# Performance work log

Hardware: AMD Instinct MI355X
Metric: run time of the kernel (lower is better)

Reference implementation:

```python
import jax, jax.numpy as jnp
import numpy as np


def _softsplat(tenIn, tenFlow):
    """Bilinear forward splatting: scatter tenIn to flow-displaced locations.
    tenIn: [N,C,H,W], tenFlow: [N,2,H,W] -> out [N,C,H,W]."""
    N, C, H, W = tenIn.shape
    dt = tenIn.dtype
    gx = jnp.arange(W, dtype=dt)[None, None, :]   # [1,1,W]
    gy = jnp.arange(H, dtype=dt)[None, :, None]   # [1,H,1]
    fx = gx + tenFlow[:, 0]                       # [N,H,W] target x
    fy = gy + tenFlow[:, 1]                       # [N,H,W] target y
    finite = jnp.isfinite(fx) & jnp.isfinite(fy)
    x0f = jnp.floor(fx)
    y0f = jnp.floor(fy)
    ix0 = x0f.astype(jnp.int32)
    iy0 = y0f.astype(jnp.int32)
    # bilinear corner weights (NW, NE, SW, SE) exactly as in the CUDA kernel
    wx1 = fx - x0f            # weight toward east
    wx0 = (x0f + 1.0) - fx    # weight toward west
    wy1 = fy - y0f            # weight toward south
    wy0 = (y0f + 1.0) - fy    # weight toward north
    corners = [
        (ix0,     iy0,     wx0 * wy0),  # NW
        (ix0 + 1, iy0,     wx1 * wy0),  # NE
        (ix0,     iy0 + 1, wx0 * wy1),  # SW
        (ix0 + 1, iy0 + 1, wx1 * wy1),  # SE
    ]
    HW = H * W
    tenIn_flat = tenIn.reshape(N, C, HW)

    def scatter_corner(ix, iy, w):
        valid = finite & (ix >= 0) & (ix < W) & (iy >= 0) & (iy < H)
        idx = jnp.where(valid, iy * W + ix, 0).reshape(N, HW)       # [N,HW]
        wv = jnp.where(valid, w, jnp.zeros_like(w)).reshape(N, 1, HW)
        vals = (tenIn_flat * wv).transpose(0, 2, 1)                 # [N,HW,C]
        seg = jax.vmap(lambda v, i: jax.ops.segment_sum(v, i, num_segments=HW))(vals, idx)
        return seg                                                   # [N,HW,C]

    out = scatter_corner(*corners[0])
    for c in corners[1:]:
        out = out + scatter_corner(*c)
    return out.transpose(0, 2, 1).reshape(N, C, H, W)


def softsplat_softmax(tenIn, tenFlow, tenMetric):
    # strMode == 'softmax': splat [tenIn * exp(metric), exp(metric)], then normalize
    w = jnp.exp(tenMetric)                          # [N,1,H,W]
    packed = jnp.concatenate([tenIn * w, w], axis=1)
    out = _softsplat(packed, tenFlow)
    norm = out[:, -1:]
    norm = jnp.where(norm == 0.0, jnp.ones_like(norm), norm)
    return out[:, :-1] / norm


def setup_inputs() -> dict:
    key = jax.random.key(0)
    k1, k2, k3 = jax.random.split(key, 3)
    N, C, H, W = 8, 64, 288, 512
    tenIn = jax.random.normal(k1, (N, C, H, W), dtype=jnp.float32)
    tenFlow = jax.random.normal(k2, (N, 2, H, W), dtype=jnp.float32)
    tenMetric = jax.random.normal(k3, (N, 1, H, W), dtype=jnp.float32)
    return {"tenIn": tenIn, "tenFlow": tenFlow, "tenMetric": tenMetric}


def reference(tenIn, tenFlow, tenMetric):
    return softsplat_softmax(tenIn, tenFlow, tenMetric)
```

## Files before the change

kernel.cpp:

```cpp
#include <hip/hip_runtime.h>
#include <hip/hip_fp16.h>
#include <math.h>

constexpr int N  = 8;
constexpr int C  = 64;
constexpr int H  = 288;
constexpr int W  = 512;
constexpr int HW = H * W;

constexpr int TW = 64, TH = 32, R = 8;
constexpr int PW = TW + 2 * R;
constexpr int PH = TH + 2 * R;
constexpr int PS = PW * PH;
constexpr int TGX = W / TW;
constexpr int TGY = H / TH;
constexpr int TILES = N * TGX * TGY;
constexpr int NOUT = TH * TW;
constexpr int K = 12;
constexpr int CCHB = 4;
constexpr int NCHUNK = C / CCHB;
constexpr int NSPLIT = 2;
constexpr int CPB = NCHUNK / NSPLIT;
constexpr int OVFCAP = 256;
constexpr int ESCCAP = 512;
constexpr int NTC = 512;
constexpr int NTG = 1024;
constexpr int GGRID = TILES * NSPLIT;

constexpr size_t CLAIM_LDS_WORDS = (size_t)NOUT * (K + 1);
constexpr size_t CLAIM_LDS_BYTES = CLAIM_LDS_WORDS * 4;

constexpr size_t WS_DEN  = 0;
constexpr size_t WS_META = WS_DEN  + (size_t)N * HW;
constexpr size_t WS_OVFC = WS_META + (size_t)TILES * NOUT * K;
constexpr size_t WS_OVFE = WS_OVFC + TILES;
constexpr size_t WS_ESCC = WS_OVFE + (size_t)TILES * OVFCAP * 2;
constexpr size_t WS_ESCE = WS_ESCC + TILES;

__device__ __forceinline__ int swz(int si) { return si ^ ((si >> 4) & 15); }

__device__ __forceinline__ unsigned packh2(float a, float b) {
    __half2 h = __floats2half2_rn(a, b);
    return *reinterpret_cast<unsigned*>(&h);
}
__device__ __forceinline__ float2 unpackh2(unsigned u) {
    __half2 h = *reinterpret_cast<__half2*>(&u);
    return __half22float2(h);
}

__global__ __launch_bounds__(NTC) void claim_kernel(
    const float* __restrict__ flow, const float* __restrict__ metric,
    unsigned* __restrict__ meta,
    unsigned* __restrict__ ovfc, unsigned* __restrict__ ovfe,
    unsigned* __restrict__ escc, unsigned* __restrict__ esce,
    float* __restrict__ den)
{
    extern __shared__ unsigned smem[];
    unsigned* cnt = smem;
    unsigned* ml  = smem + NOUT;

    for (int i = threadIdx.x; i < NOUT; i += NTC) cnt[i] = 0;
    for (int i = threadIdx.x; i < NOUT * K; i += NTC) ml[i] = 0u;
    __syncthreads();

    const int t  = blockIdx.x;
    const int n  = t / (TGX * TGY);
    const int r  = t % (TGX * TGY);
    const int Y0 = (r / TGX) * TH;
    const int X0 = (r % TGX) * TW;

    const float* fxp = flow + ((size_t)n * 2) * HW;
    const float* fyp = fxp + HW;
    const float* mp  = metric + (size_t)n * HW;
    unsigned* mt = meta + (size_t)t * NOUT * K;

    for (int si = threadIdx.x; si < PS; si += NTC) {
        int ys = Y0 - R + si / PW;
        int xs = X0 - R + si % PW;
        if ((unsigned)ys >= (unsigned)H || (unsigned)xs >= (unsigned)W) continue;
        int p = ys * W + xs;
        float fx = fxp[p] + (float)xs;
        float fy = fyp[p] + (float)ys;
        if (!(isfinite(fx) && isfinite(fy))) continue;
        float x0f = floorf(fx), y0f = floorf(fy);
        int ix0 = (int)x0f, iy0 = (int)y0f;
        int tx = ix0 - X0;
        int ty = iy0 - Y0;
        float wx1 = fx - x0f, wx0 = x0f + 1.0f - fx;
        float wy1 = fy - y0f, wy0 = y0f + 1.0f - fy;
        float wm  = __expf(mp[p]);
        int sis = swz(si);

        #define CLAIM(TYv, TXv, Wv)                                           \
            if ((unsigned)(TYv) < (unsigned)TH &&                             \
                (unsigned)(TXv) < (unsigned)TW) {                             \
                float w_ = (Wv) * wm;                                         \
                int   o_ = (TYv) * TW + (TXv);                                \
                unsigned slot = atomicAdd(&cnt[o_], 1u);                      \
                if (slot < (unsigned)K) {                                     \
                    ml[o_ * K + (int)slot] =                                  \
                        ((unsigned)__half_as_ushort(__float2half(w_)) << 16)  \
                        | (unsigned)sis;                                      \
                } else {                                                      \
                    unsigned p2 = atomicAdd(&ovfc[t], 1u);                    \
                    if (p2 < (unsigned)OVFCAP) {                              \
                        unsigned* e = ovfe + ((size_t)t * OVFCAP + p2) * 2;   \
                        e[0] = ((unsigned)o_ << 16) | (unsigned)sis;          \
                        e[1] = __float_as_uint(w_);                           \
                    }                                                         \
                }                                                             \
            }
        CLAIM(ty,     tx,     wx0 * wy0)
        CLAIM(ty,     tx + 1, wx1 * wy0)
        CLAIM(ty + 1, tx,     wx0 * wy1)
        CLAIM(ty + 1, tx + 1, wx1 * wy1)
        #undef CLAIM

        if ((unsigned)(xs - X0) < (unsigned)TW &&
            (unsigned)(ys - Y0) < (unsigned)TH) {
            int   cx[4] = { ix0, ix0 + 1, ix0,     ix0 + 1 };
            int   cy[4] = { iy0, iy0,     iy0 + 1, iy0 + 1 };
            float cw[4] = { wx0 * wy0, wx1 * wy0, wx0 * wy1, wx1 * wy1 };
            #pragma unroll
            for (int k = 0; k < 4; ++k) {
                if ((unsigned)cx[k] >= (unsigned)W ||
                    (unsigned)cy[k] >= (unsigned)H) continue;
                int tX0 = cx[k] & ~(TW - 1);
                int tY0 = cy[k] & ~(TH - 1);
                bool inpad = (xs >= tX0 - R) && (xs < tX0 + TW + R) &&
                             (ys >= tY0 - R) && (ys < tY0 + TH + R);
                if (inpad) continue;
                int tt = n * (TGX * TGY) + (tY0 >> 5) * TGX + (tX0 >> 6);
                unsigned pos = atomicAdd(&escc[tt], 1u);
                if (pos < (unsigned)ESCCAP) {
                    unsigned* e = esce + ((size_t)tt * ESCCAP + pos) * 3;
                    e[0] = (unsigned)((cy[k] - tY0) * TW + (cx[k] - tX0));
                    e[1] = (unsigned)p;
                    e[2] = __float_as_uint(cw[k] * wm);
                }
            }
        }
    }
    __syncthreads();

    const unsigned on = min(ovfc[t], (unsigned)OVFCAP);
    const unsigned* oe = ovfe + (size_t)t * OVFCAP * 2;
    for (int o = threadIdx.x; o < NOUT; o += NTC) {
        unsigned cn = min(cnt[o], (unsigned)K);
        float d = 0.0f;
        for (unsigned s = 0; s < cn; ++s)
            d += __half2float(__ushort_as_half(
                     (unsigned short)(ml[o * K + (int)s] >> 16)));
        for (unsigned i = 0; i < on; ++i)
            if ((oe[2 * i] >> 16) == (unsigned)o)
                d += __uint_as_float(oe[2 * i + 1]);
        den[(size_t)n * HW + (Y0 + o / TW) * W + X0 + o % TW] = d;
    }

    const uint4* mlv = reinterpret_cast<const uint4*>(ml);
    uint4* mtv = reinterpret_cast<uint4*>(mt);
    for (int i = threadIdx.x; i < NOUT * K / 4; i += NTC)
        mtv[i] = mlv[i];
}

__global__ __launch_bounds__(NTG, 4) void gather_kernel(
    const float* __restrict__ in, const unsigned* __restrict__ meta,
    const unsigned* __restrict__ ovfc, const unsigned* __restrict__ ovfe,
    const unsigned* __restrict__ escc, const unsigned* __restrict__ esce,
    const float* __restrict__ den, float* __restrict__ out)
{
    __shared__ uint2 val[2][PS];

    const int b0 = blockIdx.x;
    const int b  = (b0 & 7) * (GGRID / 8) + (b0 >> 3);
    const int t     = b >> 1;
    const int split = b & 1;
    const int n  = t / (TGX * TGY);
    const int r  = t % (TGX * TGY);
    const int Y0 = (r / TGX) * TH;
    const int X0 = (r % TGX) * TW;

    const unsigned on = min(ovfc[t], (unsigned)OVFCAP);
    const unsigned en = min(escc[t], (unsigned)ESCCAP);
    const unsigned* oe = ovfe + (size_t)t * OVFCAP * 2;
    const unsigned* ee = esce + (size_t)t * ESCCAP * 3;
    const unsigned* mt = meta + (size_t)t * NOUT * K;

    float inv[2];
    int   opix[2];
    #pragma unroll
    for (int k = 0; k < 2; ++k) {
        int o = threadIdx.x + k * NTG;
        opix[k] = (Y0 + o / TW) * W + X0 + o % TW;
        float d = den[(size_t)n * HW + opix[k]];
        for (unsigned i = 0; i < en; ++i)
            if (ee[3 * i] == (unsigned)o) d += __uint_as_float(ee[3 * i + 2]);
        inv[k] = (d == 0.0f) ? 1.0f : 1.0f / d;
    }

    const bool stager = threadIdx.x < PS / 4;
    int si0 = 0, sw = 0, soff = 0;
    bool ok = false;
    if (stager) {
        si0 = threadIdx.x * 4;
        int row = si0 / PW;
        int ys  = Y0 - R + row;
        int xs0 = X0 - R + (si0 - row * PW);
        ok  = (unsigned)ys < (unsigned)H && (unsigned)xs0 < (unsigned)W;
        sw  = (si0 >> 4) & 15;
        soff = ys * W + xs0;
    }
    const float* inb0 = in + ((size_t)n * C + split * CPB * CCHB) * HW;

    float4 g0 = {0,0,0,0}, g1 = g0, g2 = g0, g3 = g0;
    if (stager && ok) {
        const float* pp = inb0 + soff;
        g0 = *reinterpret_cast<const float4*>(pp);
        g1 = *reinterpret_cast<const float4*>(pp + HW);
        g2 = *reinterpret_cast<const float4*>(pp + 2 * HW);
        g3 = *reinterpret_cast<const float4*>(pp + 3 * HW);
    }
    if (stager) {
        val[0][(si0    ) ^ sw] = make_uint2(packh2(g0.x, g1.x), packh2(g2.x, g3.x));
        val[0][(si0 + 1) ^ sw] = make_uint2(packh2(g0.y, g1.y), packh2(g2.y, g3.y));
        val[0][(si0 + 2) ^ sw] = make_uint2(packh2(g0.z, g1.z), packh2(g2.z, g3.z));
        val[0][(si0 + 3) ^ sw] = make_uint2(packh2(g0.w, g1.w), packh2(g2.w, g3.w));
    }

    int cur = 0;
    for (int cc = 0; cc < CPB; ++cc) {
        __syncthreads();
        const float* inb = inb0 + (size_t)cc * CCHB * HW;

        if (cc + 1 < CPB && stager) {
            g0 = make_float4(0,0,0,0); g1 = g0; g2 = g0; g3 = g0;
            if (ok) {
                const float* pn = inb + (size_t)CCHB * HW + soff;
                g0 = *reinterpret_cast<const float4*>(pn);
                g1 = *reinterpret_cast<const float4*>(pn + HW);
                g2 = *reinterpret_cast<const float4*>(pn + 2 * HW);
                g3 = *reinterpret_cast<const float4*>(pn + 3 * HW);
            }
        }

        const uint2* vb = val[cur];
        #pragma unroll
        for (int k = 0; k < 2; ++k) {
            const int o = threadIdx.x + k * NTG;
            const uint4* mo4 = reinterpret_cast<const uint4*>(mt + (size_t)o * K);
            uint4 qa = mo4[0], qb = mo4[1], qc = mo4[2];
            unsigned mloc[K] = { qa.x, qa.y, qa.z, qa.w,
                                 qb.x, qb.y, qb.z, qb.w,
                                 qc.x, qc.y, qc.z, qc.w };

            float a0 = 0.0f, a1 = 0.0f, a2 = 0.0f, a3 = 0.0f;
            #pragma unroll
            for (int s = 0; s < K; ++s) {
                unsigned m_ = mloc[s];
                float w  = __half2float(__ushort_as_half((unsigned short)(m_ >> 16)));
                uint2 v = vb[m_ & 0xffffu];
                float2 f0 = unpackh2(v.x), f1 = unpackh2(v.y);
                a0 += w * f0.x;  a1 += w * f0.y;
                a2 += w * f1.x;  a3 += w * f1.y;
            }
            for (unsigned i = 0; i < on; ++i) {
                unsigned e0 = oe[2 * i];
                if ((e0 >> 16) == (unsigned)o) {
                    float w  = __uint_as_float(oe[2 * i + 1]);
                    uint2 v = vb[e0 & 0xffffu];
                    float2 f0 = unpackh2(v.x), f1 = unpackh2(v.y);
                    a0 += w * f0.x;  a1 += w * f0.y;
                    a2 += w * f1.x;  a3 += w * f1.y;
                }
            }
            for (unsigned i = 0; i < en; ++i) {
                if (ee[3 * i] == (unsigned)o) {
                    float w  = __uint_as_float(ee[3 * i + 2]);
                    int   ps = (int)ee[3 * i + 1];
                    a0 += w * inb[ps];
                    a1 += w * inb[ps + HW];
                    a2 += w * inb[ps + 2 * HW];
                    a3 += w * inb[ps + 3 * HW];
                }
            }
            size_t ob = ((size_t)n * C + (split * CPB + cc) * CCHB) * HW + opix[k];
            out[ob]          = a0 * inv[k];
            out[ob + HW]     = a1 * inv[k];
            out[ob + 2 * HW] = a2 * inv[k];
            out[ob + 3 * HW] = a3 * inv[k];
        }

        if (cc + 1 < CPB && stager) {
            uint2* vn = val[cur ^ 1];
            vn[(si0    ) ^ sw] = make_uint2(packh2(g0.x, g1.x), packh2(g2.x, g3.x));
            vn[(si0 + 1) ^ sw] = make_uint2(packh2(g0.y, g1.y), packh2(g2.y, g3.y));
            vn[(si0 + 2) ^ sw] = make_uint2(packh2(g0.z, g1.z), packh2(g2.z, g3.z));
            vn[(si0 + 3) ^ sw] = make_uint2(packh2(g0.w, g1.w), packh2(g2.w, g3.w));
        }
        cur ^= 1;
    }
}

extern "C" void kernel_launch(void* const* d_in, const int* in_sizes, int n_in,
                              void* d_out, int out_size, void* d_ws, size_t ws_size,
                              hipStream_t stream)
{
    const float* tenIn     = (const float*)d_in[0];
    const float* tenFlow   = (const float*)d_in[1];
    const float* tenMetric = (const float*)d_in[2];
    float* out = (float*)d_out;

    unsigned* ws  = (unsigned*)d_ws;
    float*    den = (float*)(ws + WS_DEN);
    unsigned* meta = ws + WS_META;
    unsigned* ovfc = ws + WS_OVFC;
    unsigned* ovfe = ws + WS_OVFE;
    unsigned* escc = ws + WS_ESCC;
    unsigned* esce = ws + WS_ESCE;

    hipFuncSetAttribute(reinterpret_cast<const void*>(claim_kernel),
                        hipFuncAttributeMaxDynamicSharedMemorySize,
                        (int)CLAIM_LDS_BYTES);

    hipMemsetAsync(ovfc, 0, TILES * sizeof(unsigned), stream);
    hipMemsetAsync(escc, 0, TILES * sizeof(unsigned), stream);

    claim_kernel<<<TILES, NTC, CLAIM_LDS_BYTES, stream>>>(
        tenFlow, tenMetric, meta, ovfc, ovfe, escc, esce, den);
    gather_kernel<<<GGRID, NTG, 0, stream>>>(tenIn, meta, ovfc, ovfe,
                                             escc, esce, den, out);
}
```

Baseline: 230.1 us.

## Halve gather block size and drop LDS double buffering for occupancy

The gather kernel now runs 512 threads per block instead of 1024, and each thread handles four output pixels instead of two. The double-buffered LDS staging with register prefetch is replaced by a single buffer. Each channel chunk is now staged cooperatively in a loop and bracketed by two barriers. This halves LDS per block and removes the prefetch registers, so more blocks can be resident and hide latency. In exchange, the explicit overlap of global loads for the next chunk with compute on the current one is lost.

```diff
diff --git a/kernel.cpp b/kernel.cpp
--- a/kernel.cpp
+++ b/kernel.cpp
@@ -24,7 +24,8 @@
 constexpr int OVFCAP = 256;
 constexpr int ESCCAP = 512;
 constexpr int NTC = 512;
-constexpr int NTG = 1024;
+constexpr int NTG = 512;
+constexpr int OPT = NOUT / NTG;
 constexpr int GGRID = TILES * NSPLIT;
 
 constexpr size_t CLAIM_LDS_WORDS = (size_t)NOUT * (K + 1);
@@ -169,7 +170,7 @@
     const unsigned* __restrict__ escc, const unsigned* __restrict__ esce,
     const float* __restrict__ den, float* __restrict__ out)
 {
-    __shared__ uint2 val[2][PS];
+    __shared__ uint2 val[PS];
 
     const int b0 = blockIdx.x;
     const int b  = (b0 & 7) * (GGRID / 8) + (b0 >> 3);
@@ -179,6 +180,7 @@
     const int r  = t % (TGX * TGY);
     const int Y0 = (r / TGX) * TH;
     const int X0 = (r % TGX) * TW;
+    const int tid = threadIdx.x;
 
     const unsigned on = min(ovfc[t], (unsigned)OVFCAP);
     const unsigned en = min(escc[t], (unsigned)ESCCAP);
@@ -186,11 +188,11 @@
     const unsigned* ee = esce + (size_t)t * ESCCAP * 3;
     const unsigned* mt = meta + (size_t)t * NOUT * K;
 
-    float inv[2];
-    int   opix[2];
+    float inv[OPT];
+    int   opix[OPT];
     #pragma unroll
-    for (int k = 0; k < 2; ++k) {
-        int o = threadIdx.x + k * NTG;
+    for (int k = 0; k < OPT; ++k) {
+        int o = tid + k * NTG;
         opix[k] = (Y0 + o / TW) * W + X0 + o % TW;
         float d = den[(size_t)n * HW + opix[k]];
         for (unsigned i = 0; i < en; ++i)
@@ -198,55 +200,36 @@
         inv[k] = (d == 0.0f) ? 1.0f : 1.0f / d;
     }
 
-    const bool stager = threadIdx.x < PS / 4;
-    int si0 = 0, sw = 0, soff = 0;
-    bool ok = false;
-    if (stager) {
-        si0 = threadIdx.x * 4;
-        int row = si0 / PW;
-        int ys  = Y0 - R + row;
-        int xs0 = X0 - R + (si0 - row * PW);
-        ok  = (unsigned)ys < (unsigned)H && (unsigned)xs0 < (unsigned)W;
-        sw  = (si0 >> 4) & 15;
-        soff = ys * W + xs0;
-    }
     const float* inb0 = in + ((size_t)n * C + split * CPB * CCHB) * HW;
 
-    float4 g0 = {0,0,0,0}, g1 = g0, g2 = g0, g3 = g0;
-    if (stager && ok) {
-        const float* pp = inb0 + soff;
-        g0 = *reinterpret_cast<const float4*>(pp);
-        g1 = *reinterpret_cast<const float4*>(pp + HW);
-        g2 = *reinterpret_cast<const float4*>(pp + 2 * HW);
-        g3 = *reinterpret_cast<const float4*>(pp + 3 * HW);
-    }
-    if (stager) {
-        val[0][(si0    ) ^ sw] = make_uint2(packh2(g0.x, g1.x), packh2(g2.x, g3.x));
-        val[0][(si0 + 1) ^ sw] = make_uint2(packh2(g0.y, g1.y), packh2(g2.y, g3.y));
-        val[0][(si0 + 2) ^ sw] = make_uint2(packh2(g0.z, g1.z), packh2(g2.z, g3.z));
-        val[0][(si0 + 3) ^ sw] = make_uint2(packh2(g0.w, g1.w), packh2(g2.w, g3.w));
-    }
-
-    int cur = 0;
     for (int cc = 0; cc < CPB; ++cc) {
+        const float* inb = inb0 + (size_t)cc * CCHB * HW;
         __syncthreads();
-        const float* inb = inb0 + (size_t)cc * CCHB * HW;
-
-        if (cc + 1 < CPB && stager) {
-            g0 = make_float4(0,0,0,0); g1 = g0; g2 = g0; g3 = g0;
+        for (int q = tid; q < PS / 4; q += NTG) {
+            int si0 = q * 4;
+            int row = si0 / PW;
+            int ys  = Y0 - R + row;
+            int xs0 = X0 - R + (si0 - row * PW);
+            bool ok = (unsigned)ys < (unsigned)H && (unsigned)xs0 < (unsigned)W;
+            float4 g0 = {0,0,0,0}, g1 = g0, g2 = g0, g3 = g0;
             if (ok) {
-                const float* pn = inb + (size_t)CCHB * HW + soff;
-                g0 = *reinterpret_cast<const float4*>(pn);
-                g1 = *reinterpret_cast<const float4*>(pn + HW);
-                g2 = *reinterpret_cast<const float4*>(pn + 2 * HW);
-                g3 = *reinterpret_cast<const float4*>(pn + 3 * HW);
-            }
+                const float* pp = inb + ys * W + xs0;
+                g0 = *reinterpret_cast<const float4*>(pp);
+                g1 = *reinterpret_cast<const float4*>(pp + HW);
+                g2 = *reinterpret_cast<const float4*>(pp + 2 * HW);
+                g3 = *reinterpret_cast<const float4*>(pp + 3 * HW);
+            }
+            int sw = (si0 >> 4) & 15;
+            val[(si0    ) ^ sw] = make_uint2(packh2(g0.x, g1.x), packh2(g2.x, g3.x));
+            val[(si0 + 1) ^ sw] = make_uint2(packh2(g0.y, g1.y), packh2(g2.y, g3.y));
+            val[(si0 + 2) ^ sw] = make_uint2(packh2(g0.z, g1.z), packh2(g2.z, g3.z));
+            val[(si0 + 3) ^ sw] = make_uint2(packh2(g0.w, g1.w), packh2(g2.w, g3.w));
         }
-
-        const uint2* vb = val[cur];
+        __syncthreads();
+
         #pragma unroll
-        for (int k = 0; k < 2; ++k) {
-            const int o = threadIdx.x + k * NTG;
+        for (int k = 0; k < OPT; ++k) {
+            const int o = tid + k * NTG;
             const uint4* mo4 = reinterpret_cast<const uint4*>(mt + (size_t)o * K);
             uint4 qa = mo4[0], qb = mo4[1], qc = mo4[2];
             unsigned mloc[K] = { qa.x, qa.y, qa.z, qa.w,
@@ -258,7 +241,7 @@
             for (int s = 0; s < K; ++s) {
                 unsigned m_ = mloc[s];
                 float w  = __half2float(__ushort_as_half((unsigned short)(m_ >> 16)));
-                uint2 v = vb[m_ & 0xffffu];
+                uint2 v = val[m_ & 0xffffu];
                 float2 f0 = unpackh2(v.x), f1 = unpackh2(v.y);
                 a0 += w * f0.x;  a1 += w * f0.y;
                 a2 += w * f1.x;  a3 += w * f1.y;
@@ -267,7 +250,7 @@
                 unsigned e0 = oe[2 * i];
                 if ((e0 >> 16) == (unsigned)o) {
                     float w  = __uint_as_float(oe[2 * i + 1]);
-                    uint2 v = vb[e0 & 0xffffu];
+                    uint2 v = val[e0 & 0xffffu];
                     float2 f0 = unpackh2(v.x), f1 = unpackh2(v.y);
                     a0 += w * f0.x;  a1 += w * f0.y;
                     a2 += w * f1.x;  a3 += w * f1.y;
@@ -289,15 +272,6 @@
             out[ob + 2 * HW] = a2 * inv[k];
             out[ob + 3 * HW] = a3 * inv[k];
         }
-
-        if (cc + 1 < CPB && stager) {
-            uint2* vn = val[cur ^ 1];
-            vn[(si0    ) ^ sw] = make_uint2(packh2(g0.x, g1.x), packh2(g2.x, g3.x));
-            vn[(si0 + 1) ^ sw] = make_uint2(packh2(g0.y, g1.y), packh2(g2.y, g3.y));
-            vn[(si0 + 2) ^ sw] = make_uint2(packh2(g0.z, g1.z), packh2(g2.z, g3.z));
-            vn[(si0 + 3) ^ sw] = make_uint2(packh2(g0.w, g1.w), packh2(g2.w, g3.w));
-        }
-        cur ^= 1;
     }
 }
 
```

Result: slower. 588.1 us (+155.7%).
